# Kernel optimization log

Measured on AMD Instinct MI355X. Metric: run time of the kernel, lower is better.

## Reference

```python
import jax, jax.numpy as jnp
import numpy as np

N = 67108864  # 64M elements, ~256 MB fp32


def setup_inputs() -> dict:
    key = jax.random.key(0)
    x = jax.random.normal(key, (N,), dtype=jnp.float32)
    return {"x": x, "bins": 256, "min": -4, "max": 4}


def reference(x, bins, min, max):
    # Faithful jnp translation of torch.histc:
    #   bin width = (max - min) / bins
    #   values in [min, max] are counted; x == max falls in the last bin;
    #   values outside the range are dropped. Output dtype matches input (float).
    lo = jnp.float32(min)
    hi = jnp.float32(max)
    width = (hi - lo) / bins
    idx = jnp.floor((x - lo) / width).astype(jnp.int32)
    # right edge is inclusive -> goes to last bin
    idx = jnp.clip(idx, 0, bins - 1)
    in_range = (x >= lo) & (x <= hi)
    w = jnp.where(in_range, jnp.float32(1.0), jnp.float32(0.0))
    hist = jnp.zeros((bins,), dtype=jnp.float32).at[idx].add(w)
    return hist
```

## Files before the change

### kernel.cpp

```cpp
#include <hip/hip_runtime.h>

#define NBINS 256
#define NCOPY 16
#define CSTRIDE 257

__global__ void zero_out_kernel(float* __restrict__ out) {
    out[threadIdx.x] = 0.0f;
}

__global__ __launch_bounds__(256) void hist_kernel(const float* __restrict__ x,
                                                   float* __restrict__ out,
                                                   int n) {
    __shared__ int lh[NCOPY * CSTRIDE];
    const int tid = threadIdx.x;
    int* __restrict__ myh = &lh[(tid >> 4) * CSTRIDE];

    for (int i = tid; i < NCOPY * CSTRIDE; i += 256)
        lh[i] = 0;
    __syncthreads();

    const int gid    = blockIdx.x * 256 + tid;
    const int stride = gridDim.x * 256;
    const int n4     = n >> 2;
    const float4* __restrict__ x4 = (const float4*)x;

#define PROC(f) do {                                    \
        float _t = ((f) + 4.0f) * 32.0f;                \
        if ((f) >= -4.0f && (f) <= 4.0f) {              \
            int _b = (int)_t;                           \
            _b = _b > (NBINS - 1) ? (NBINS - 1) : _b;   \
            atomicAdd(&myh[_b], 1);                     \
        }                                               \
    } while (0)

    int i = gid;
    for (; i + stride < n4; i += 2 * stride) {
        float4 a = x4[i];
        float4 b = x4[i + stride];
        PROC(a.x); PROC(a.y); PROC(a.z); PROC(a.w);
        PROC(b.x); PROC(b.y); PROC(b.z); PROC(b.w);
    }
    if (i < n4) {
        float4 a = x4[i];
        PROC(a.x); PROC(a.y); PROC(a.z); PROC(a.w);
    }

    for (int j = (n4 << 2) + gid; j < n; j += stride) {
        float f = x[j];
        PROC(f);
    }
#undef PROC

    __syncthreads();

    int s = 0;
    #pragma unroll
    for (int c = 0; c < NCOPY; ++c)
        s += lh[c * CSTRIDE + tid];
    if (s)
        atomicAdd(&out[tid], (float)s);
}

extern "C" void kernel_launch(void* const* d_in, const int* in_sizes, int n_in,
                              void* d_out, int out_size, void* d_ws, size_t ws_size,
                              hipStream_t stream) {
    const float* x = (const float*)d_in[0];
    float* out = (float*)d_out;
    const int n = in_sizes[0];

    zero_out_kernel<<<1, NBINS, 0, stream>>>(out);

    int n4 = n >> 2;
    int blocks = (n4 + 255) / 256;
    if (blocks > 2048) blocks = 2048;
    if (blocks < 1) blocks = 1;
    hist_kernel<<<blocks, 256, 0, stream>>>(x, out, n);
}
```

Baseline: 88.39 us.

## Use per-thread byte histograms in LDS with run caching and a separate reduce pass

Replaces the shared-memory histogram copies updated with atomics by a private 8-bit histogram per thread in LDS. A cached current-bin counter lets repeated hits on the same bin skip the LDS write, and out-of-range values go to a padding slot. Each block sums its byte counters with packed 32-bit reads and writes a per-block partial histogram to workspace, and a second kernel reduces the partials into the output. This is meant to remove LDS atomic contention on the skewed bins, but the 8-bit counters could overflow if the workspace cap forces each thread to process more elements than planned.

```diff
diff --git a/kernel.cpp b/kernel.cpp
--- a/kernel.cpp
+++ b/kernel.cpp
@@ -1,64 +1,108 @@
 #include <hip/hip_runtime.h>
 
 #define NBINS 256
-#define NCOPY 16
-#define CSTRIDE 257
+#define TPB 128
+#define RSTRIDE 260
+#define RSTRIDE_DW 65
 
 __global__ void zero_out_kernel(float* __restrict__ out) {
     out[threadIdx.x] = 0.0f;
 }
 
-__global__ __launch_bounds__(256) void hist_kernel(const float* __restrict__ x,
-                                                   float* __restrict__ out,
+__global__ __launch_bounds__(TPB) void hist_kernel(const float* __restrict__ x,
+                                                   float* __restrict__ ws,
                                                    int n) {
-    __shared__ int lh[NCOPY * CSTRIDE];
+    __shared__ unsigned char lh[TPB * RSTRIDE];
+    unsigned int* lh32 = (unsigned int*)lh;
     const int tid = threadIdx.x;
-    int* __restrict__ myh = &lh[(tid >> 4) * CSTRIDE];
+    unsigned char* __restrict__ reg = &lh[tid * RSTRIDE];
 
-    for (int i = tid; i < NCOPY * CSTRIDE; i += 256)
-        lh[i] = 0;
+    for (int i = tid; i < TPB * RSTRIDE_DW; i += TPB) lh32[i] = 0;
     __syncthreads();
 
-    const int gid    = blockIdx.x * 256 + tid;
-    const int stride = gridDim.x * 256;
+    const int gid    = blockIdx.x * TPB + tid;
+    const int stride = gridDim.x * TPB;
     const int n4     = n >> 2;
     const float4* __restrict__ x4 = (const float4*)x;
 
-#define PROC(f) do {                                    \
-        float _t = ((f) + 4.0f) * 32.0f;                \
-        if ((f) >= -4.0f && (f) <= 4.0f) {              \
-            int _b = (int)_t;                           \
-            _b = _b > (NBINS - 1) ? (NBINS - 1) : _b;   \
-            atomicAdd(&myh[_b], 1);                     \
-        }                                               \
-    } while (0)
+    int cur_b = 256;
+    unsigned int cur_v = 0;
+
+#define PROC(f) {                                              \
+        float _s  = (f) + 4.0f;                                \
+        float _t  = _s * 32.0f;                                \
+        bool  _ok = ((f) >= -4.0f) & ((f) <= 4.0f);            \
+        int   _b  = (int)_t;                                   \
+        _b = _b > 255 ? 255 : _b;                              \
+        _b = _ok ? _b : 256;                                   \
+        unsigned int _nv = reg[_b];                            \
+        reg[cur_b] = (unsigned char)(cur_v + 1u);              \
+        cur_v = (_b == cur_b) ? cur_v + 1u : _nv;              \
+        cur_b = _b;                                            \
+    }
 
     int i = gid;
-    for (; i + stride < n4; i += 2 * stride) {
+    for (; i + 3 * stride < n4; i += 4 * stride) {
         float4 a = x4[i];
         float4 b = x4[i + stride];
-        PROC(a.x); PROC(a.y); PROC(a.z); PROC(a.w);
-        PROC(b.x); PROC(b.y); PROC(b.z); PROC(b.w);
+        float4 c = x4[i + 2 * stride];
+        float4 d = x4[i + 3 * stride];
+        PROC(a.x) PROC(a.y) PROC(a.z) PROC(a.w)
+        PROC(b.x) PROC(b.y) PROC(b.z) PROC(b.w)
+        PROC(c.x) PROC(c.y) PROC(c.z) PROC(c.w)
+        PROC(d.x) PROC(d.y) PROC(d.z) PROC(d.w)
     }
-    if (i < n4) {
+    for (; i < n4; i += stride) {
         float4 a = x4[i];
-        PROC(a.x); PROC(a.y); PROC(a.z); PROC(a.w);
+        PROC(a.x) PROC(a.y) PROC(a.z) PROC(a.w)
     }
-
     for (int j = (n4 << 2) + gid; j < n; j += stride) {
         float f = x[j];
-        PROC(f);
+        PROC(f)
     }
 #undef PROC
+    reg[cur_b] = (unsigned char)(cur_v + 1u);
 
     __syncthreads();
 
-    int s = 0;
-    #pragma unroll
-    for (int c = 0; c < NCOPY; ++c)
-        s += lh[c * CSTRIDE + tid];
-    if (s)
-        atomicAdd(&out[tid], (float)s);
+    const int c = tid & 63;
+    const int h = tid >> 6;
+    unsigned s0 = 0, s1 = 0, s2 = 0, s3 = 0;
+    for (int k = 0; k < 64; ++k) {
+        unsigned v = lh32[(h * 64 + k) * RSTRIDE_DW + c];
+        s0 += v & 0xFFu;
+        s1 += (v >> 8) & 0xFFu;
+        s2 += (v >> 16) & 0xFFu;
+        s3 += v >> 24;
+    }
+    __syncthreads();
+    if (h == 1) {
+        lh32[c * 4 + 0] = s0;
+        lh32[c * 4 + 1] = s1;
+        lh32[c * 4 + 2] = s2;
+        lh32[c * 4 + 3] = s3;
+    }
+    __syncthreads();
+    if (h == 0) {
+        s0 += lh32[c * 4 + 0];
+        s1 += lh32[c * 4 + 1];
+        s2 += lh32[c * 4 + 2];
+        s3 += lh32[c * 4 + 3];
+        float4 o;
+        o.x = (float)s0; o.y = (float)s1; o.z = (float)s2; o.w = (float)s3;
+        ((float4*)ws)[blockIdx.x * 64 + c] = o;
+    }
+}
+
+__global__ __launch_bounds__(256) void reduce_kernel(const float* __restrict__ ws,
+                                                     float* __restrict__ out,
+                                                     int nblk) {
+    const int tid = threadIdx.x;
+    float s = 0.0f;
+    for (int i = blockIdx.x; i < nblk; i += gridDim.x)
+        s += ws[i * NBINS + tid];
+    if (s != 0.0f)
+        atomicAdd(&out[tid], s);
 }
 
 extern "C" void kernel_launch(void* const* d_in, const int* in_sizes, int n_in,
@@ -66,13 +110,18 @@
                               hipStream_t stream) {
     const float* x = (const float*)d_in[0];
     float* out = (float*)d_out;
+    float* ws  = (float*)d_ws;
     const int n = in_sizes[0];
 
+    const int n4 = n >> 2;
+    long long want = ((long long)n4 + (long long)TPB * 32 - 1) / ((long long)TPB * 32);
+    int blocks = (int)(want < 1 ? 1 : want);
+    long long ws_cap = (long long)(ws_size / (NBINS * sizeof(float)));
+    if (blocks > ws_cap) blocks = (int)ws_cap;
+
+    hist_kernel<<<blocks, TPB, 0, stream>>>(x, ws, n);
     zero_out_kernel<<<1, NBINS, 0, stream>>>(out);
 
-    int n4 = n >> 2;
-    int blocks = (n4 + 255) / 256;
-    if (blocks > 2048) blocks = 2048;
-    if (blocks < 1) blocks = 1;
-    hist_kernel<<<blocks, 256, 0, stream>>>(x, out, n);
+    int rblocks = blocks < 64 ? blocks : 64;
+    reduce_kernel<<<rblocks, NBINS, 0, stream>>>(ws, out, blocks);
 }
```

Measured after the change: 94.16 us. 1.07x slower.

## Use per-wave histogram copies, branchless binning, nontemporal 4-way unrolled loads

Applied to the files above, without the earlier changes.

Cuts the shared histogram replicas from 16 per block (one per 16 threads) to 4 (one per 64-thread wavefront), with a padded stride. Out-of-range values now go to a dummy bin 256 instead of taking a branch. Each loop iteration issues four nontemporal float4 loads instead of two. Fewer copies shrink zeroing and reduction work, but more threads now contend on the same LDS atomics, which could serialize when values cluster near the center of the normal distribution.

```diff
diff --git a/kernel.cpp b/kernel.cpp
--- a/kernel.cpp
+++ b/kernel.cpp
@@ -1,62 +1,66 @@
 #include <hip/hip_runtime.h>
 
 #define NBINS 256
-#define NCOPY 16
-#define CSTRIDE 257
+#define TPB 256
+#define NCOPY 4
+#define CSTRIDE 264
+
+typedef float f32x4 __attribute__((ext_vector_type(4)));
 
 __global__ void zero_out_kernel(float* __restrict__ out) {
     out[threadIdx.x] = 0.0f;
 }
 
-__global__ __launch_bounds__(256) void hist_kernel(const float* __restrict__ x,
+__global__ __launch_bounds__(TPB) void hist_kernel(const float* __restrict__ x,
                                                    float* __restrict__ out,
                                                    int n) {
     __shared__ int lh[NCOPY * CSTRIDE];
     const int tid = threadIdx.x;
-    int* __restrict__ myh = &lh[(tid >> 4) * CSTRIDE];
+    int* __restrict__ myh = &lh[(tid >> 6) * CSTRIDE];
 
-    for (int i = tid; i < NCOPY * CSTRIDE; i += 256)
+    for (int i = tid; i < NCOPY * CSTRIDE; i += TPB)
         lh[i] = 0;
     __syncthreads();
 
-    const int gid    = blockIdx.x * 256 + tid;
-    const int stride = gridDim.x * 256;
+    const int gid    = blockIdx.x * TPB + tid;
+    const int stride = gridDim.x * TPB;
     const int n4     = n >> 2;
-    const float4* __restrict__ x4 = (const float4*)x;
+    const f32x4* __restrict__ x4 = (const f32x4*)x;
 
-#define PROC(f) do {                                    \
-        float _t = ((f) + 4.0f) * 32.0f;                \
-        if ((f) >= -4.0f && (f) <= 4.0f) {              \
-            int _b = (int)_t;                           \
-            _b = _b > (NBINS - 1) ? (NBINS - 1) : _b;   \
-            atomicAdd(&myh[_b], 1);                     \
-        }                                               \
-    } while (0)
+#define PROC(f) {                                        \
+        float _t = ((f) + 4.0f) * 32.0f;                 \
+        int   _b = (int)_t;                              \
+        _b = _b > 255 ? 255 : _b;                        \
+        bool _ok = ((f) >= -4.0f) & ((f) <= 4.0f);       \
+        _b = _ok ? _b : 256;                             \
+        atomicAdd(&myh[_b], 1);                          \
+    }
 
     int i = gid;
-    for (; i + stride < n4; i += 2 * stride) {
-        float4 a = x4[i];
-        float4 b = x4[i + stride];
-        PROC(a.x); PROC(a.y); PROC(a.z); PROC(a.w);
-        PROC(b.x); PROC(b.y); PROC(b.z); PROC(b.w);
+    for (; i + 3 * stride < n4; i += 4 * stride) {
+        f32x4 a = __builtin_nontemporal_load(&x4[i]);
+        f32x4 b = __builtin_nontemporal_load(&x4[i + stride]);
+        f32x4 c = __builtin_nontemporal_load(&x4[i + 2 * stride]);
+        f32x4 d = __builtin_nontemporal_load(&x4[i + 3 * stride]);
+        PROC(a.x) PROC(a.y) PROC(a.z) PROC(a.w)
+        PROC(b.x) PROC(b.y) PROC(b.z) PROC(b.w)
+        PROC(c.x) PROC(c.y) PROC(c.z) PROC(c.w)
+        PROC(d.x) PROC(d.y) PROC(d.z) PROC(d.w)
     }
-    if (i < n4) {
-        float4 a = x4[i];
-        PROC(a.x); PROC(a.y); PROC(a.z); PROC(a.w);
+    for (; i < n4; i += stride) {
+        f32x4 a = __builtin_nontemporal_load(&x4[i]);
+        PROC(a.x) PROC(a.y) PROC(a.z) PROC(a.w)
     }
-
     for (int j = (n4 << 2) + gid; j < n; j += stride) {
         float f = x[j];
-        PROC(f);
+        PROC(f)
     }
 #undef PROC
 
     __syncthreads();
 
-    int s = 0;
-    #pragma unroll
-    for (int c = 0; c < NCOPY; ++c)
-        s += lh[c * CSTRIDE + tid];
+    int s = lh[0 * CSTRIDE + tid] + lh[1 * CSTRIDE + tid] +
+            lh[2 * CSTRIDE + tid] + lh[3 * CSTRIDE + tid];
     if (s)
         atomicAdd(&out[tid], (float)s);
 }
@@ -71,8 +75,7 @@
     zero_out_kernel<<<1, NBINS, 0, stream>>>(out);
 
     int n4 = n >> 2;
-    int blocks = (n4 + 255) / 256;
-    if (blocks > 2048) blocks = 2048;
-    if (blocks < 1) blocks = 1;
-    hist_kernel<<<blocks, 256, 0, stream>>>(x, out, n);
+    long long want = ((long long)n4 + (long long)TPB * 4 - 1) / ((long long)TPB * 4);
+    int blocks = (int)(want < 1 ? 1 : (want > 2048 ? 2048 : want));
+    hist_kernel<<<blocks, TPB, 0, stream>>>(x, out, n);
 }
```

Result: faster. 79.29 us (-10.3%).
